# Kernel tuning notes

Measured on AMD Instinct MI355X. Metric: run time of the kernel, lower is better.

The kernel has to match this reference:

```python
import jax, jax.numpy as jnp
import numpy as np

EPS = 1e-6

def _exp_map0(v):
    # v: [..., D] tangent at origin with v[...,0]==0
    sp = v[..., 1:]
    n = jnp.sqrt(jnp.clip(jnp.sum(sp * sp, -1, keepdims=True), EPS))
    return jnp.concatenate([jnp.cosh(n), jnp.sinh(n) / n * sp], -1)

def _log_map0(x):
    x0 = x[..., :1]
    sp = x[..., 1:]
    n = jnp.sqrt(jnp.clip(jnp.sum(sp * sp, -1, keepdims=True), EPS))
    d = jnp.arccosh(jnp.clip(x0, 1.0 + EPS))
    return jnp.concatenate([jnp.zeros_like(x0), d / n * sp], -1)

def _pt_to_origin(x, v):
    # parallel transport v from T_x to T_o, o=(1,0,...,0):
    # PT(v) = v + <o,v>_L / (1 - <x,o>_L) * (x + o);  <o,v>_L=-v0, <x,o>_L=-x0
    coef = -v[..., :1] / (1.0 + x[..., :1])
    x_plus_o = jnp.concatenate([x[..., :1] + 1.0, x[..., 1:]], -1)
    return v + coef * x_plus_o

def _linear(h, W, b):
    # torch nn.Linear: h @ W.T + b, W: [out, in]
    return jnp.einsum('bne,de->bnd', h, W) + b

def setup_inputs() -> dict:
    key = jax.random.key(0)
    ks = jax.random.split(key, 8)
    B, N, d = 8, 2048, 256
    # manifold points via exp_map0 of small tangents
    t = jax.random.normal(ks[0], (B, N, d), jnp.float32) * 0.1
    x = _exp_map0(jnp.pad(t, ((0, 0), (0, 0), (1, 0))))
    # tangent velocity at x: project random u onto T_x (add <x,u>_L * x since <x,x>_L=-1)
    u = jax.random.normal(ks[1], (B, N, d + 1), jnp.float32) * 0.1
    xu = jnp.sum(x * u, -1, keepdims=True) - 2.0 * x[..., :1] * u[..., :1]  # Lorentz inner
    x_vel = u + xu * x
    s = 1.0 / np.sqrt(d)
    Wq = jax.random.normal(ks[2], (d, d), jnp.float32) * s
    Wk = jax.random.normal(ks[3], (d, d), jnp.float32) * s
    Wv = jax.random.normal(ks[4], (d, d), jnp.float32) * s
    bq = jnp.zeros((d,), jnp.float32)
    bk = jnp.zeros((d,), jnp.float32)
    bv = jnp.zeros((d,), jnp.float32)
    tau = jnp.ones((1,), jnp.float32)
    return {"x": x, "x_vel": x_vel, "Wq": Wq, "bq": bq, "Wk": Wk, "bk": bk,
            "Wv": Wv, "bv": bv, "tau": tau}

def reference(x, x_vel, Wq, bq, Wk, bk, Wv, bv, tau):
    lambda_penalty = 1.0
    log_x = _log_map0(x)
    x_tan = log_x[..., 1:]                                   # [B,N,d]
    q_s = _linear(x_tan, Wq, bq)
    k_s = _linear(x_tan, Wk, bk)
    v_s = _linear(x_tan, Wv, bv)
    pad = lambda h: jnp.pad(h, ((0, 0), (0, 0), (1, 0)))
    q = _exp_map0(pad(q_s))                                  # [B,N,D]
    k = _exp_map0(pad(k_s))
    log_v = pad(v_s)
    vel0 = _pt_to_origin(x, x_vel)
    q_vel = _linear(vel0[..., 1:], Wq, bq)                   # [B,N,d]
    k_vel = _linear(vel0[..., 1:], Wk, bk)
    # pairwise Lorentz distance: <q,k>_L = sum(q*k) - 2*q0*k0
    inner = jnp.einsum('bnd,bmd->bnm', q, k) \
            - 2.0 * q[..., 0][:, :, None] * k[..., 0][:, None, :]
    d_L = jnp.arccosh(jnp.clip(-inner, 1.0 + EPS))           # [B,N,N]
    q_sq = jnp.sum(q_vel * q_vel, -1)                        # [B,N]
    k_sq = jnp.sum(k_vel * k_vel, -1)
    qk = jnp.einsum('bnd,bmd->bnm', q_vel, k_vel)
    pen = jnp.clip(q_sq[:, :, None] + k_sq[:, None, :] - 2.0 * qk, 0.0)
    tau_c = jnp.clip(tau, 0.001)[0]
    logits = -(1.0 / tau_c) * d_L ** 2 - lambda_penalty * pen
    attn = jax.nn.softmax(logits, axis=-1)                   # [B,N,N]
    agg = jnp.einsum('bnm,bmd->bnd', attn, log_v)
    z = _exp_map0(agg)
    return z, attn, x_tan
```

## Files before the change

kernel.cpp:

```cpp
#include <hip/hip_runtime.h>
#include <math.h>

#define BB 8
#define NN 2048
#define DD 256
#define TT (BB*NN)
#define DP1 257
#define EPSF 1e-6f

typedef _Float16 f16;
typedef __attribute__((ext_vector_type(8))) _Float16 f16x8;
typedef __attribute__((ext_vector_type(4))) float f32x4;

#define BAR() asm volatile("s_barrier" ::: "memory")
#define WAIT_VM(N) asm volatile("s_waitcnt vmcnt(" #N ")" ::: "memory")
#define WAIT_LGKM0() asm volatile("s_waitcnt lgkmcnt(0)" ::: "memory")

__device__ __forceinline__ f32x4 mfma16(f16x8 a, f16x8 b, f32x4 c) {
  return __builtin_amdgcn_mfma_f32_16x16x32_f16(a, b, c, 0, 0, 0);
}
__device__ __forceinline__ void gll16(const f16* g, f16* l) {
  __builtin_amdgcn_global_load_lds(
      (const __attribute__((address_space(1))) void*)g,
      (__attribute__((address_space(3))) void*)l, 16, 0, 0);
}

__device__ __forceinline__ float wave_sum(float v) {
#pragma unroll
  for (int m = 1; m < 64; m <<= 1) v += __shfl_xor(v, m);
  return v;
}

__global__ __launch_bounds__(256) void prep_kernel(
    const float* __restrict__ x, const float* __restrict__ xv,
    float* __restrict__ xtan, f16* __restrict__ xtan_h, f16* __restrict__ vel0_h) {
  const int w = threadIdx.x >> 6, l = threadIdx.x & 63;
  const int tok = blockIdx.x * 4 + w;
  const float* xr = x  + (size_t)tok * DP1;
  const float* vr = xv + (size_t)tok * DP1;
  float x0 = xr[0];
  float sp[4];
  float ss = 0.f;
#pragma unroll
  for (int j = 0; j < 4; j++) { sp[j] = xr[1 + l + 64 * j]; ss = fmaf(sp[j], sp[j], ss); }
  ss = wave_sum(ss);
  float n  = sqrtf(fmaxf(ss, EPSF));
  float dd = acoshf(fmaxf(x0, 1.f + EPSF));
  float scl = dd / n;
  float coef = -vr[0] / (1.f + x0);
  const size_t base = (size_t)tok * DD;
#pragma unroll
  for (int j = 0; j < 4; j++) {
    float xt = scl * sp[j];
    xtan[base + l + 64 * j] = xt;
    xtan_h[base + l + 64 * j] = (f16)xt;
    vel0_h[base + l + 64 * j] = (f16)(vr[1 + l + 64 * j] + coef * sp[j]);
  }
}

__global__ __launch_bounds__(256) void wcast_kernel(
    const float* __restrict__ Wq, const float* __restrict__ Wk,
    const float* __restrict__ Wv, f16* __restrict__ Wh) {
  const int m = blockIdx.y;
  const int i = blockIdx.x * 256 + threadIdx.x;
  const float* W = (m == 0) ? Wq : ((m == 1) ? Wk : Wv);
  Wh[(size_t)m * DD * DD + i] = (f16)W[i];
}

__global__ __launch_bounds__(256, 2) void gemm_mfma(
    const f16* __restrict__ xtan_h, const f16* __restrict__ vel0_h,
    const f16* __restrict__ Wh,
    f16* __restrict__ qh, f16* __restrict__ kh, f16* __restrict__ vT,
    f16* __restrict__ qvh, f16* __restrict__ kvh,
    const float* __restrict__ bq, const float* __restrict__ bk,
    const float* __restrict__ bv) {
  __shared__ __align__(16) f16 sA[2 * 4096];
  __shared__ __align__(16) f16 sB[2 * 4096];
  const int tid = threadIdx.x;
  const int bm = blockIdx.x * 128;
  const int bn = blockIdx.y * 128;
  const int seg = bn >> 8;
  const int w = tid >> 6, l = tid & 63;
  const int wr = w >> 1, wc = w & 1;
  f32x4 acc[4][4] = {};
  const f16* Ab = ((seg < 3) ? xtan_h : vel0_h) + (size_t)bm * DD;
  const f16* Bb = Wh + (size_t)((seg < 3) ? bn : (bn - 768)) * DD;

  auto stage = [&](int nx) {
    const int half = nx & 1, k0 = nx * 32;
#pragma unroll
    for (int p = 0; p < 2; p++) {
      int u = tid + p * 256;
      int row = u >> 2;
      int q = (u & 3) ^ ((u >> 3) & 3);
      size_t go = (size_t)row * DD + k0 + q * 8;
      size_t lb = (size_t)half * 4096 + (size_t)(w * 64 + p * 256) * 8;
      gll16(Ab + go, sA + lb);
      gll16(Bb + go, sB + lb);
    }
  };

  stage(0);
  const int fq = ((l >> 4) ^ ((l >> 1) & 3)) * 8;
  for (int kt = 0; kt < 8; ++kt) {
    if (kt < 7) { stage(kt + 1); WAIT_VM(4); }
    else        { WAIT_VM(0); }
    BAR();
    const int co = (kt & 1) * 4096;
    f16x8 af[4], bf[4];
#pragma unroll
    for (int i = 0; i < 4; i++)
      af[i] = *(const f16x8*)(sA + co + (wr * 64 + i * 16 + (l & 15)) * 32 + fq);
#pragma unroll
    for (int j = 0; j < 4; j++)
      bf[j] = *(const f16x8*)(sB + co + (wc * 64 + j * 16 + (l & 15)) * 32 + fq);
#pragma unroll
    for (int i = 0; i < 4; i++)
#pragma unroll
      for (int j = 0; j < 4; j++)
        acc[i][j] = mfma16(af[i], bf[j], acc[i][j]);
    BAR();
  }

  f16* optr = (seg == 0) ? qh : (seg == 1) ? kh : (seg == 2) ? vT : (seg == 3) ? qvh : kvh;
  const float* bias = (seg == 0 || seg == 3) ? bq : (seg == 1 || seg == 4) ? bk : bv;
  const int ot = (seg == 2) ? 1 : 0;
  const int rl = (l >> 4) * 4, cl = l & 15;
#pragma unroll
  for (int i = 0; i < 4; i++) {
#pragma unroll
    for (int j = 0; j < 4; j++) {
      const int col = (bn & 255) + wc * 64 + j * 16 + cl;
      const float bvv = bias[col];
      const int row0 = bm + wr * 64 + i * 16 + rl;
      if (ot == 0) {
#pragma unroll
        for (int r = 0; r < 4; r++)
          optr[(size_t)(row0 + r) * DD + col] = (f16)(acc[i][j][r] + bvv);
      } else {
        __align__(8) f16 tmp[4];
#pragma unroll
        for (int r = 0; r < 4; r++) tmp[r] = (f16)(acc[i][j][r] + bvv);
        f16* dst = optr + ((size_t)((row0 >> 11) * DD + col)) * NN + (row0 & (NN - 1));
        *(uint2*)dst = *(const uint2*)tmp;
      }
    }
  }
}

__global__ __launch_bounds__(256) void scale_kernel(
    f16* __restrict__ qh, f16* __restrict__ kh,
    const f16* __restrict__ qvh, const f16* __restrict__ kvh,
    float* __restrict__ q0, float* __restrict__ k0v,
    float* __restrict__ q_sq, float* __restrict__ k_sq) {
  const int w = threadIdx.x >> 6, l = threadIdx.x & 63;
  const int tok = blockIdx.x * 4 + w;
  const size_t base = (size_t)tok * DD;
  float q[4], k[4];
  float sq = 0.f, sk = 0.f, svq = 0.f, svk = 0.f;
#pragma unroll
  for (int j = 0; j < 4; j++) {
    size_t off = base + l + 64 * j;
    q[j] = (float)qh[off];
    k[j] = (float)kh[off];
    float qv = (float)qvh[off], kv = (float)kvh[off];
    sq = fmaf(q[j], q[j], sq);
    sk = fmaf(k[j], k[j], sk);
    svq = fmaf(qv, qv, svq);
    svk = fmaf(kv, kv, svk);
  }
  sq = wave_sum(sq); sk = wave_sum(sk);
  svq = wave_sum(svq); svk = wave_sum(svk);
  float nq = sqrtf(fmaxf(sq, EPSF));
  float nk = sqrtf(fmaxf(sk, EPSF));
  float scq = sinhf(nq) / nq, sck = sinhf(nk) / nk;
#pragma unroll
  for (int j = 0; j < 4; j++) {
    size_t off = base + l + 64 * j;
    qh[off] = (f16)(q[j] * scq);
    kh[off] = (f16)(k[j] * sck);
  }
  if (l == 0) {
    q0[tok] = coshf(nq);
    k0v[tok] = coshf(nk);
    q_sq[tok] = svq;
    k_sq[tok] = svk;
  }
}

__global__ __launch_bounds__(256, 2) void logits_mfma(
    const f16* __restrict__ qh, const f16* __restrict__ kh,
    const f16* __restrict__ qvh, const f16* __restrict__ kvh,
    const float* __restrict__ q0a, const float* __restrict__ k0a,
    const float* __restrict__ qsqa, const float* __restrict__ ksqa,
    const float* __restrict__ tau, float* __restrict__ attn,
    float* __restrict__ psum) {
  __shared__ __align__(16) f16 sQ[2*4096], sK[2*4096], sQv[2*4096], sKv[2*4096];
  const int tid = threadIdx.x;
  const int bid = blockIdx.x;
  const int b = bid & 7;
  const int bq = ((bid >> 3) & 15) * 128;
  const int kti = bid >> 7;
  const int bk = kti * 128;
  const size_t tb = (size_t)b * NN;
  const f16* Q  = qh  + (tb + bq) * DD;
  const f16* Kp = kh  + (tb + bk) * DD;
  const f16* Qv = qvh + (tb + bq) * DD;
  const f16* Kv = kvh + (tb + bk) * DD;
  const int w = tid >> 6, l = tid & 63;
  const int wr = w >> 1, wc = w & 1;
  f32x4 accq[4][4] = {}, accv[4][4] = {};

  auto stage = [&](int nx) {
    const int half = nx & 1, k0 = nx * 32;
#pragma unroll
    for (int p = 0; p < 2; p++) {
      int u = tid + p * 256;
      int row = u >> 2;
      int q = (u & 3) ^ ((u >> 3) & 3);
      size_t go = (size_t)row * DD + k0 + q * 8;
      size_t lb = (size_t)half * 4096 + (size_t)(w * 64 + p * 256) * 8;
      gll16(Kp + go, sK  + lb);
      gll16(Q  + go, sQ  + lb);
      gll16(Kv + go, sKv + lb);
      gll16(Qv + go, sQv + lb);
    }
  };

  stage(0);
  const int fq = ((l >> 4) ^ ((l >> 1) & 3)) * 8;
  for (int kt = 0; kt < 8; ++kt) {
    if (kt < 7) { stage(kt + 1); WAIT_VM(8); }
    else        { WAIT_VM(0); }
    BAR();
    const int co = (kt & 1) * 4096;
    {
      f16x8 ak[4], bqf[4];
#pragma unroll
      for (int i = 0; i < 4; i++)
        ak[i] = *(const f16x8*)(sK + co + (wr * 64 + i * 16 + (l & 15)) * 32 + fq);
#pragma unroll
      for (int j = 0; j < 4; j++)
        bqf[j] = *(const f16x8*)(sQ + co + (wc * 64 + j * 16 + (l & 15)) * 32 + fq);
#pragma unroll
      for (int i = 0; i < 4; i++)
#pragma unroll
        for (int j = 0; j < 4; j++)
          accq[i][j] = mfma16(ak[i], bqf[j], accq[i][j]);
    }
    {
      f16x8 ak[4], bqf[4];
#pragma unroll
      for (int i = 0; i < 4; i++)
        ak[i] = *(const f16x8*)(sKv + co + (wr * 64 + i * 16 + (l & 15)) * 32 + fq);
#pragma unroll
      for (int j = 0; j < 4; j++)
        bqf[j] = *(const f16x8*)(sQv + co + (wc * 64 + j * 16 + (l & 15)) * 32 + fq);
#pragma unroll
      for (int i = 0; i < 4; i++)
#pragma unroll
        for (int j = 0; j < 4; j++)
          accv[i][j] = mfma16(ak[i], bqf[j], accv[i][j]);
    }
    BAR();
  }

  const int rl = (l >> 4) * 4, cl = l & 15;
  const float invt = 1.f / fmaxf(tau[0], 1e-3f);
  const float cc = invt * 0.4804530139182014f;
  float q0r[4], qsr[4];
  float4 k0c[4], ksc[4];
#pragma unroll
  for (int j = 0; j < 4; j++) {
    const int qq = bq + wc * 64 + j * 16 + cl;
    q0r[j] = q0a[tb + qq];
    qsr[j] = qsqa[tb + qq];
  }
#pragma unroll
  for (int i = 0; i < 4; i++) {
    const int kk = bk + wr * 64 + i * 16 + rl;
    k0c[i] = *(const float4*)(k0a + tb + kk);
    ksc[i] = *(const float4*)(ksqa + tb + kk);
  }
  const size_t obase = (size_t)b * NN * NN;
#pragma unroll
  for (int j = 0; j < 4; j++) {
    const int qq = bq + wc * 64 + j * 16 + cl;
    const float q0 = q0r[j], qs = qsr[j];
    float es = 0.f;
#pragma unroll
    for (int i = 0; i < 4; i++) {
      const int kk = bk + wr * 64 + i * 16 + rl;
      const float* k0p = (const float*)&k0c[i];
      const float* ksp = (const float*)&ksc[i];
      float4 o;
      float* op = (float*)&o;
#pragma unroll
      for (int r = 0; r < 4; r++) {
        float xv = fmaxf(fmaf(q0, k0p[r], -accq[i][j][r]), 1.f + EPSF);
        float s = sqrtf(fmaf(xv, xv, -1.f));
        float lg = __log2f(xv + s);
        float pen = fmaxf(fmaf(-2.f, accv[i][j][r], qs + ksp[r]), 0.f);
        float lo = fmaf(-cc * lg, lg, -pen);
        float ex = __expf(lo);
        op[r] = ex;
        es += ex;
      }
      *(float4*)(attn + obase + (size_t)qq * NN + kk) = o;
    }
    es += __shfl_xor(es, 16);
    es += __shfl_xor(es, 32);
    if ((l >> 4) == 0)
      psum[((size_t)(b * 16 + kti) * 2 + wr) * NN + qq] = es;
  }
}

__global__ __launch_bounds__(256, 2) void pv_fused(
    const float* __restrict__ psum, const f16* __restrict__ vT,
    float* __restrict__ attn, float* __restrict__ z) {
  __shared__ __align__(16) f16 sP[2][32 * 32];
  __shared__ __align__(16) f16 sV[3][256 * 32];
  __shared__ float invs_l[32];
  __shared__ float zsum[4][32];
  __shared__ float zsc[32];
  const int tid = threadIdx.x;
  const int bid = blockIdx.x;
  const int b = bid & 7;
  const int row0 = (bid >> 3) * 32;
  const int w = tid >> 6, l = tid & 63;
  float* slab = attn + ((size_t)b * NN + row0) * NN;
  const f16* Vb = vT + (size_t)b * DD * NN;

  if (tid < 32) {
    float s = 0.f;
#pragma unroll 4
    for (int p = 0; p < 32; p++) s += psum[((size_t)b * 32 + p) * NN + row0 + tid];
    invs_l[tid] = 1.f / s;
  }
  __syncthreads();
  const int prow = tid >> 3, pm4 = tid & 7;
  const float myinv = invs_l[prow];
  const int fq = ((l >> 4) ^ ((l >> 1) & 3)) * 8;
  const int spo = prow * 32 + ((pm4 >> 1) ^ ((prow >> 1) & 3)) * 8 + (pm4 & 1) * 4;
  f32x4 acc[2][4] = {};
  float4 pA, pB;

#define STAGEV(nx, vb) do { const int m0_ = (nx) * 32;                          \
    _Pragma("unroll")                                                           \
    for (int p_ = 0; p_ < 4; p_++) {                                            \
      int u_ = tid + p_ * 256;                                                  \
      int d_ = u_ >> 2;                                                         \
      int q_ = (u_ & 3) ^ ((u_ >> 3) & 3);                                      \
      gll16(Vb + (size_t)d_ * NN + m0_ + q_ * 8,                                \
            (f16*)&sV[vb][0] + (size_t)(w * 64 + p_ * 256) * 8);                \
    } } while (0)
#define LOADP(nx, reg) do {                                                     \
    reg = *(const float4*)(slab + (size_t)prow * NN + (nx) * 32 + pm4 * 4);     \
  } while (0)
#define USEP(nx, reg) do {                                                      \
    float e0_ = reg.x * myinv, e1_ = reg.y * myinv;                             \
    float e2_ = reg.z * myinv, e3_ = reg.w * myinv;                             \
    float4 ov_ = {e0_, e1_, e2_, e3_};                                          \
    *(float4*)(slab + (size_t)prow * NN + (nx) * 32 + pm4 * 4) = ov_;           \
    __align__(8) f16 tmp_[4] = {(f16)e0_, (f16)e1_, (f16)e2_, (f16)e3_};        \
    *(uint2*)(&sP[(nx) & 1][spo]) = *(const uint2*)tmp_;                        \
  } while (0)
#define COMPUTE(t, vb) do {                                                     \
    f16x8 af_[2], bf_[4];                                                       \
    _Pragma("unroll")                                                           \
    for (int i_ = 0; i_ < 2; i_++)                                              \
      af_[i_] = *(const f16x8*)(&sP[(t) & 1][(i_ * 16 + (l & 15)) * 32 + fq]);  \
    _Pragma("unroll")                                                           \
    for (int j_ = 0; j_ < 4; j_++)                                              \
      bf_[j_] = *(const f16x8*)((const f16*)&sV[vb][0] +                        \
                                (w * 64 + j_ * 16 + (l & 15)) * 32 + fq);       \
    _Pragma("unroll")                                                           \
    for (int i_ = 0; i_ < 2; i_++)                                              \
      _Pragma("unroll")                                                         \
      for (int j_ = 0; j_ < 4; j_++)                                            \
        acc[i_][j_] = mfma16(af_[i_], bf_[j_], acc[i_][j_]);                    \
  } while (0)

  STAGEV(0, 0); LOADP(0, pA);
  STAGEV(1, 1); LOADP(1, pB);
  WAIT_VM(5);
  USEP(0, pA);
  WAIT_LGKM0();
  BAR();

  int vb0 = 0;
  for (int tt = 0; tt < 32; ++tt) {
    {
      const int t = 2 * tt;
      const int vb_t = vb0;
      const int vb_s = (vb0 + 2 > 2) ? vb0 - 1 : vb0 + 2;
      if (t < 62) { STAGEV(t + 2, vb_s); LOADP(t + 2, pA); WAIT_VM(5); }
      else        { WAIT_VM(1); }
      if (t < 63) USEP(t + 1, pB);
      COMPUTE(t, vb_t);
      WAIT_LGKM0();
      BAR();
    }
    {
      const int t = 2 * tt + 1;
      const int vb_t = (vb0 + 1 > 2) ? vb0 - 2 : vb0 + 1;
      const int vb_s = vb0;
      if (t < 62)      { STAGEV(t + 2, vb_s); LOADP(t + 2, pB); WAIT_VM(5); }
      else if (t == 62){ WAIT_VM(1); }
      else             { WAIT_VM(0); }
      if (t < 63) USEP(t + 1, pA);
      COMPUTE(t, vb_t);
      WAIT_LGKM0();
      BAR();
    }
    vb0 = (vb0 + 2 > 2) ? vb0 - 1 : vb0 + 2;
  }
#undef STAGEV
#undef LOADP
#undef USEP
#undef COMPUTE

  const int rl4 = (l >> 4) * 4, cl = l & 15;
  float s2[2][4];
#pragma unroll
  for (int i = 0; i < 2; i++)
#pragma unroll
    for (int r = 0; r < 4; r++) {
      float s = 0.f;
#pragma unroll
      for (int j = 0; j < 4; j++) s = fmaf(acc[i][j][r], acc[i][j][r], s);
#pragma unroll
      for (int m = 1; m < 16; m <<= 1) s += __shfl_xor(s, m);
      s2[i][r] = s;
    }
  if (cl == 0) {
#pragma unroll
    for (int i = 0; i < 2; i++)
#pragma unroll
      for (int r = 0; r < 4; r++)
        zsum[w][i * 16 + rl4 + r] = s2[i][r];
  }
  __syncthreads();
  if (tid < 32) {
    float n2 = zsum[0][tid] + zsum[1][tid] + zsum[2][tid] + zsum[3][tid];
    float nn = sqrtf(fmaxf(n2, EPSF));
    zsc[tid] = sinhf(nn) / nn;
    z[(size_t)(b * NN + row0 + tid) * DP1] = coshf(nn);
  }
  __syncthreads();
#pragma unroll
  for (int i = 0; i < 2; i++)
#pragma unroll
    for (int r = 0; r < 4; r++) {
      const int row = i * 16 + rl4 + r;
      const float sc = zsc[row];
      const size_t zb = (size_t)(b * NN + row0 + row) * DP1 + 1;
#pragma unroll
      for (int j = 0; j < 4; j++)
        z[zb + w * 64 + j * 16 + cl] = acc[i][j][r] * sc;
    }
}

extern "C" void kernel_launch(void* const* d_in, const int* in_sizes, int n_in,
                              void* d_out, int out_size, void* d_ws, size_t ws_size,
                              hipStream_t stream) {
  const float* x   = (const float*)d_in[0];
  const float* xv  = (const float*)d_in[1];
  const float* Wq  = (const float*)d_in[2];
  const float* bq  = (const float*)d_in[3];
  const float* Wk  = (const float*)d_in[4];
  const float* bk  = (const float*)d_in[5];
  const float* Wv  = (const float*)d_in[6];
  const float* bv  = (const float*)d_in[7];
  const float* tau = (const float*)d_in[8];
  float* out = (float*)d_out;
  char* ws = (char*)d_ws;

  const size_t TD2 = (size_t)TT * DD * 2;

  f16*   qh     = (f16*)(ws);
  f16*   kh     = (f16*)(ws + TD2);
  f16*   qvh    = (f16*)(ws + 2 * TD2);
  f16*   kvh    = (f16*)(ws + 3 * TD2);
  f16*   vT     = (f16*)(ws + 4 * TD2);
  f16*   xtan_h = (f16*)(ws + 5 * TD2);
  f16*   vel0_h = (f16*)(ws + 6 * TD2);
  f16*   Wh     = (f16*)(ws + 7 * TD2);
  float* psum   = (float*)(ws + 7 * TD2 + 3 * DD * DD * 2);
  float* q0     = psum + (size_t)BB * 32 * NN;
  float* k0v    = q0 + TT;
  float* q_sq   = q0 + 2 * TT;
  float* k_sq   = q0 + 3 * TT;

  float* z_out    = out;
  float* attn_out = out + (size_t)TT * DP1;
  float* xtan_out = attn_out + (size_t)BB * NN * NN;

  prep_kernel<<<TT / 4, 256, 0, stream>>>(x, xv, xtan_out, xtan_h, vel0_h);
  wcast_kernel<<<dim3(DD * DD / 256, 3), 256, 0, stream>>>(Wq, Wk, Wv, Wh);

  gemm_mfma<<<dim3(TT / 128, 10), 256, 0, stream>>>(
      xtan_h, vel0_h, Wh, qh, kh, vT, qvh, kvh, bq, bk, bv);

  scale_kernel<<<TT / 4, 256, 0, stream>>>(qh, kh, qvh, kvh, q0, k0v, q_sq, k_sq);

  logits_mfma<<<NN / 128 * NN / 128 * BB, 256, 0, stream>>>(
      qh, kh, qvh, kvh, q0, k0v, q_sq, k_sq, tau, attn_out, psum);

  pv_fused<<<NN / 32 * BB, 256, 0, stream>>>(psum, vT, attn_out, z_out);
}
```

Before: 205.6 us.

## Use nontemporal loads/stores, split QK/vel staging, and raise MFMA priority

Output writes (attn, xtan, z) and the attn slab re-read/normalize pass now use nontemporal loads and stores, so streaming data bypasses cache retention. The logits kernel splits its staging into separate K/Q and Kv/Qv phases with their own waits and barriers, so the first MFMA block can start before the velocity tiles arrive. s_setprio wraps the MFMA loops in the GEMM kernels to favour the matrix work. Risks include extra barriers per iteration and nontemporal hints hurting the normalize pass, which reads back attn data written just before.

```diff
diff --git a/kernel.cpp b/kernel.cpp
--- a/kernel.cpp
+++ b/kernel.cpp
@@ -23,6 +23,13 @@
   __builtin_amdgcn_global_load_lds(
       (const __attribute__((address_space(1))) void*)g,
       (__attribute__((address_space(3))) void*)l, 16, 0, 0);
+}
+
+__device__ __forceinline__ void nt_store4(float* p, f32x4 v) {
+  __builtin_nontemporal_store(v, (f32x4*)p);
+}
+__device__ __forceinline__ f32x4 nt_load4(const float* p) {
+  return __builtin_nontemporal_load((const f32x4*)p);
 }
 
 __device__ __forceinline__ float wave_sum(float v) {
@@ -52,7 +59,7 @@
 #pragma unroll
   for (int j = 0; j < 4; j++) {
     float xt = scl * sp[j];
-    xtan[base + l + 64 * j] = xt;
+    __builtin_nontemporal_store(xt, &xtan[base + l + 64 * j]);
     xtan_h[base + l + 64 * j] = (f16)xt;
     vel0_h[base + l + 64 * j] = (f16)(vr[1 + l + 64 * j] + coef * sp[j]);
   }
@@ -114,11 +121,13 @@
 #pragma unroll
     for (int j = 0; j < 4; j++)
       bf[j] = *(const f16x8*)(sB + co + (wc * 64 + j * 16 + (l & 15)) * 32 + fq);
+    __builtin_amdgcn_s_setprio(1);
 #pragma unroll
     for (int i = 0; i < 4; i++)
 #pragma unroll
       for (int j = 0; j < 4; j++)
         acc[i][j] = mfma16(af[i], bf[j], acc[i][j]);
+    __builtin_amdgcn_s_setprio(0);
     BAR();
   }
 
@@ -211,7 +220,7 @@
   const int wr = w >> 1, wc = w & 1;
   f32x4 accq[4][4] = {}, accv[4][4] = {};
 
-  auto stage = [&](int nx) {
+  auto stageKQ = [&](int nx) {
     const int half = nx & 1, k0 = nx * 32;
 #pragma unroll
     for (int p = 0; p < 2; p++) {
@@ -220,47 +229,67 @@
       int q = (u & 3) ^ ((u >> 3) & 3);
       size_t go = (size_t)row * DD + k0 + q * 8;
       size_t lb = (size_t)half * 4096 + (size_t)(w * 64 + p * 256) * 8;
-      gll16(Kp + go, sK  + lb);
-      gll16(Q  + go, sQ  + lb);
+      gll16(Kp + go, sK + lb);
+      gll16(Q  + go, sQ + lb);
+    }
+  };
+  auto stageVv = [&](int nx) {
+    const int half = nx & 1, k0 = nx * 32;
+#pragma unroll
+    for (int p = 0; p < 2; p++) {
+      int u = tid + p * 256;
+      int row = u >> 2;
+      int q = (u & 3) ^ ((u >> 3) & 3);
+      size_t go = (size_t)row * DD + k0 + q * 8;
+      size_t lb = (size_t)half * 4096 + (size_t)(w * 64 + p * 256) * 8;
       gll16(Kv + go, sKv + lb);
       gll16(Qv + go, sQv + lb);
     }
   };
 
-  stage(0);
+  stageKQ(0);
+  stageVv(0);
   const int fq = ((l >> 4) ^ ((l >> 1) & 3)) * 8;
   for (int kt = 0; kt < 8; ++kt) {
-    if (kt < 7) { stage(kt + 1); WAIT_VM(8); }
+    const int co = (kt & 1) * 4096;
+    if (kt < 7) { stageKQ(kt + 1); WAIT_VM(8); }
+    else        { WAIT_VM(4); }
+    BAR();
+    {
+      f16x8 ak[4], bqf[4];
+#pragma unroll
+      for (int i = 0; i < 4; i++)
+        ak[i] = *(const f16x8*)(sK + co + (wr * 64 + i * 16 + (l & 15)) * 32 + fq);
+#pragma unroll
+      for (int j = 0; j < 4; j++)
+        bqf[j] = *(const f16x8*)(sQ + co + (wc * 64 + j * 16 + (l & 15)) * 32 + fq);
+      __builtin_amdgcn_s_setprio(1);
+#pragma unroll
+      for (int i = 0; i < 4; i++)
+#pragma unroll
+        for (int j = 0; j < 4; j++)
+          accq[i][j] = mfma16(ak[i], bqf[j], accq[i][j]);
+      __builtin_amdgcn_s_setprio(0);
+    }
+    BAR();
+    if (kt < 7) { stageVv(kt + 1); WAIT_VM(8); }
     else        { WAIT_VM(0); }
     BAR();
-    const int co = (kt & 1) * 4096;
     {
       f16x8 ak[4], bqf[4];
 #pragma unroll
       for (int i = 0; i < 4; i++)
-        ak[i] = *(const f16x8*)(sK + co + (wr * 64 + i * 16 + (l & 15)) * 32 + fq);
-#pragma unroll
-      for (int j = 0; j < 4; j++)
-        bqf[j] = *(const f16x8*)(sQ + co + (wc * 64 + j * 16 + (l & 15)) * 32 + fq);
-#pragma unroll
-      for (int i = 0; i < 4; i++)
-#pragma unroll
-        for (int j = 0; j < 4; j++)
-          accq[i][j] = mfma16(ak[i], bqf[j], accq[i][j]);
-    }
-    {
-      f16x8 ak[4], bqf[4];
-#pragma unroll
-      for (int i = 0; i < 4; i++)
         ak[i] = *(const f16x8*)(sKv + co + (wr * 64 + i * 16 + (l & 15)) * 32 + fq);
 #pragma unroll
       for (int j = 0; j < 4; j++)
         bqf[j] = *(const f16x8*)(sQv + co + (wc * 64 + j * 16 + (l & 15)) * 32 + fq);
+      __builtin_amdgcn_s_setprio(1);
 #pragma unroll
       for (int i = 0; i < 4; i++)
 #pragma unroll
         for (int j = 0; j < 4; j++)
           accv[i][j] = mfma16(ak[i], bqf[j], accv[i][j]);
+      __builtin_amdgcn_s_setprio(0);
     }
     BAR();
   }
@@ -269,7 +298,7 @@
   const float invt = 1.f / fmaxf(tau[0], 1e-3f);
   const float cc = invt * 0.4804530139182014f;
   float q0r[4], qsr[4];
-  float4 k0c[4], ksc[4];
+  f32x4 k0c[4], ksc[4];
 #pragma unroll
   for (int j = 0; j < 4; j++) {
     const int qq = bq + wc * 64 + j * 16 + cl;
@@ -279,8 +308,8 @@
 #pragma unroll
   for (int i = 0; i < 4; i++) {
     const int kk = bk + wr * 64 + i * 16 + rl;
-    k0c[i] = *(const float4*)(k0a + tb + kk);
-    ksc[i] = *(const float4*)(ksqa + tb + kk);
+    k0c[i] = *(const f32x4*)(k0a + tb + kk);
+    ksc[i] = *(const f32x4*)(ksqa + tb + kk);
   }
   const size_t obase = (size_t)b * NN * NN;
 #pragma unroll
@@ -291,22 +320,19 @@
 #pragma unroll
     for (int i = 0; i < 4; i++) {
       const int kk = bk + wr * 64 + i * 16 + rl;
-      const float* k0p = (const float*)&k0c[i];
-      const float* ksp = (const float*)&ksc[i];
-      float4 o;
-      float* op = (float*)&o;
+      f32x4 o;
 #pragma unroll
       for (int r = 0; r < 4; r++) {
-        float xv = fmaxf(fmaf(q0, k0p[r], -accq[i][j][r]), 1.f + EPSF);
+        float xv = fmaxf(fmaf(q0, k0c[i][r], -accq[i][j][r]), 1.f + EPSF);
         float s = sqrtf(fmaf(xv, xv, -1.f));
         float lg = __log2f(xv + s);
-        float pen = fmaxf(fmaf(-2.f, accv[i][j][r], qs + ksp[r]), 0.f);
+        float pen = fmaxf(fmaf(-2.f, accv[i][j][r], qs + ksc[i][r]), 0.f);
         float lo = fmaf(-cc * lg, lg, -pen);
         float ex = __expf(lo);
-        op[r] = ex;
+        o[r] = ex;
         es += ex;
       }
-      *(float4*)(attn + obase + (size_t)qq * NN + kk) = o;
+      nt_store4(attn + obase + (size_t)qq * NN + kk, o);
     }
     es += __shfl_xor(es, 16);
     es += __shfl_xor(es, 32);
@@ -343,7 +369,7 @@
   const int fq = ((l >> 4) ^ ((l >> 1) & 3)) * 8;
   const int spo = prow * 32 + ((pm4 >> 1) ^ ((prow >> 1) & 3)) * 8 + (pm4 & 1) * 4;
   f32x4 acc[2][4] = {};
-  float4 pA, pB;
+  f32x4 pA, pB;
 
 #define STAGEV(nx, vb) do { const int m0_ = (nx) * 32;                          \
     _Pragma("unroll")                                                           \
@@ -355,13 +381,13 @@
             (f16*)&sV[vb][0] + (size_t)(w * 64 + p_ * 256) * 8);                \
     } } while (0)
 #define LOADP(nx, reg) do {                                                     \
-    reg = *(const float4*)(slab + (size_t)prow * NN + (nx) * 32 + pm4 * 4);     \
+    reg = nt_load4(slab + (size_t)prow * NN + (nx) * 32 + pm4 * 4);             \
   } while (0)
 #define USEP(nx, reg) do {                                                      \
-    float e0_ = reg.x * myinv, e1_ = reg.y * myinv;                             \
-    float e2_ = reg.z * myinv, e3_ = reg.w * myinv;                             \
-    float4 ov_ = {e0_, e1_, e2_, e3_};                                          \
-    *(float4*)(slab + (size_t)prow * NN + (nx) * 32 + pm4 * 4) = ov_;           \
+    float e0_ = reg[0] * myinv, e1_ = reg[1] * myinv;                           \
+    float e2_ = reg[2] * myinv, e3_ = reg[3] * myinv;                           \
+    f32x4 ov_ = {e0_, e1_, e2_, e3_};                                           \
+    nt_store4(slab + (size_t)prow * NN + (nx) * 32 + pm4 * 4, ov_);             \
     __align__(8) f16 tmp_[4] = {(f16)e0_, (f16)e1_, (f16)e2_, (f16)e3_};        \
     *(uint2*)(&sP[(nx) & 1][spo]) = *(const uint2*)tmp_;                        \
   } while (0)
@@ -445,7 +471,7 @@
     float n2 = zsum[0][tid] + zsum[1][tid] + zsum[2][tid] + zsum[3][tid];
     float nn = sqrtf(fmaxf(n2, EPSF));
     zsc[tid] = sinhf(nn) / nn;
-    z[(size_t)(b * NN + row0 + tid) * DP1] = coshf(nn);
+    __builtin_nontemporal_store(coshf(nn), &z[(size_t)(b * NN + row0 + tid) * DP1]);
   }
   __syncthreads();
 #pragma unroll
@@ -457,7 +483,7 @@
       const size_t zb = (size_t)(b * NN + row0 + row) * DP1 + 1;
 #pragma unroll
       for (int j = 0; j < 4; j++)
-        z[zb + w * 64 + j * 16 + cl] = acc[i][j][r] * sc;
+        __builtin_nontemporal_store(acc[i][j][r] * sc, &z[zb + w * 64 + j * 16 + cl]);
     }
 }
 
```

Result: slower. 248.5 us (+20.9%).
